# Kernel optimization log

Hardware: AMD Instinct MI355X
Metric: run time of the kernel (lower is better)

The kernel has to match this reference:

```python
import jax, jax.numpy as jnp
import numpy as np

N = 50000
E = 800000
IN = 128
HEADS = 4
C = 32  # out_features per head
HC = HEADS * C


def setup_inputs() -> dict:
    key = jax.random.key(0)
    ks = jax.random.split(key, 10)
    s_in = 1.0 / np.sqrt(IN)
    x = jax.random.normal(ks[0], (N, IN), dtype=jnp.float32)
    edge_index = jax.random.randint(ks[1], (2, E), 0, N, dtype=jnp.int64)
    Wq = jax.random.normal(ks[2], (IN, HC), dtype=jnp.float32) * s_in
    bq = jnp.zeros((HC,), dtype=jnp.float32)
    Wk = jax.random.normal(ks[3], (IN, HC), dtype=jnp.float32) * s_in
    bk = jnp.zeros((HC,), dtype=jnp.float32)
    Wv = jax.random.normal(ks[4], (IN, HC), dtype=jnp.float32) * s_in
    bv = jnp.zeros((HC,), dtype=jnp.float32)
    Wskip = jax.random.normal(ks[5], (IN, HC), dtype=jnp.float32) * s_in
    bskip = jnp.zeros((HC,), dtype=jnp.float32)
    return {"x": x, "edge_index": edge_index, "Wq": Wq, "bq": bq,
            "Wk": Wk, "bk": bk, "Wv": Wv, "bv": bv,
            "Wskip": Wskip, "bskip": bskip}


def reference(x, edge_index, Wq, bq, Wk, bk, Wv, bv, Wskip, bskip):
    src = edge_index[0]  # message source j
    dst = edge_index[1]  # message target i

    q = (x @ Wq + bq).reshape(N, HEADS, C)
    k = (x @ Wk + bk).reshape(N, HEADS, C)
    v = (x @ Wv + bv).reshape(N, HEADS, C)

    # per-edge attention logits: [E, H]
    logits = jnp.einsum('ehc,ehc->eh', q[dst], k[src]) / jnp.sqrt(
        jnp.asarray(C, dtype=x.dtype))

    # segment softmax over incoming edges of each target node
    seg_max = jax.ops.segment_max(logits, dst, num_segments=N)
    seg_max = jnp.where(jnp.isfinite(seg_max), seg_max, 0.0)
    expd = jnp.exp(logits - seg_max[dst])
    seg_sum = jax.ops.segment_sum(expd, dst, num_segments=N)
    alpha = expd / (seg_sum[dst] + 1e-16)  # [E, H]

    # scatter-add weighted values: [N, H, C]
    msgs = alpha[:, :, None] * v[src]
    out = jax.ops.segment_sum(msgs, dst, num_segments=N)
    out = out.reshape(N, HC) + (x @ Wskip + bskip)  # root/skip connection

    # LeakyReLU(negative_slope=0.2)
    return jnp.where(out >= 0, out, 0.2 * out)
```

## Files before the change

kernel.cpp:

```cpp
#include <hip/hip_runtime.h>

#define N_NODES 50000
#define E_EDGES 800000
#define IN_F 128
#define HC 128
#define ROWTILES 3125
#define GEMM_BLOCKS 500
#define HIST_BLOCKS 1563
#define CAP 64

typedef __attribute__((ext_vector_type(8))) short short8;
typedef __attribute__((ext_vector_type(4))) float floatx4;

__device__ __forceinline__ unsigned short f2bf(float f) {
    union { float f; unsigned u; } x; x.f = f;
    unsigned r = x.u + 0x7FFF + ((x.u >> 16) & 1);
    return (unsigned short)(r >> 16);
}
__device__ __forceinline__ float bflo(unsigned u) {
    union { unsigned u; float f; } c; c.u = u << 16; return c.f;
}
__device__ __forceinline__ float bfhi(unsigned u) {
    union { unsigned u; float f; } c; c.u = u & 0xFFFF0000u; return c.f;
}

__global__ __launch_bounds__(512) void gemm_hist(
    const float* __restrict__ x,
    const float* __restrict__ Wq, const float* __restrict__ Wk,
    const float* __restrict__ Wv, const float* __restrict__ Ws,
    const float* __restrict__ bq, const float* __restrict__ bk,
    const float* __restrict__ bv, const float* __restrict__ bs,
    unsigned short* __restrict__ q, unsigned short* __restrict__ k,
    unsigned short* __restrict__ v, float* __restrict__ out,
    const int* __restrict__ src, const int* __restrict__ dst,
    int* __restrict__ cnt, int* __restrict__ ssrc)
{
    if (blockIdx.x >= GEMM_BLOCKS) {
        int e = (blockIdx.x - GEMM_BLOCKS) * 512 + threadIdx.x;
        if (e < E_EDGES) {
            int d = dst[e];
            int r = atomicAdd(&cnt[d], 1);
            if (r < CAP) ssrc[(size_t)d * CAP + r] = src[e];
        }
        return;
    }
    __shared__ float As[16][132];
    __shared__ unsigned short Ep[3][16][136];

    const int tid = threadIdx.x;
    const int wv = tid >> 6;
    const int lane = tid & 63;
    const int cg = wv >> 1, hf = wv & 1;
    const int l16 = lane & 15, kh = lane >> 4;

    const float* Wsec = cg == 0 ? Wq : cg == 1 ? Wk : cg == 2 ? Wv : Ws;
    const float* bsec = cg == 0 ? bq : cg == 1 ? bk : cg == 2 ? bv : bs;

    short8 breg[4][4];
    float bias_[4];
#pragma unroll
    for (int n = 0; n < 4; n++) {
        const int col = (hf * 4 + n) * 16 + l16;
        bias_[n] = bsec[col];
#pragma unroll
        for (int ks = 0; ks < 4; ks++) {
            short8 bb;
#pragma unroll
            for (int j = 0; j < 8; j++)
                bb[j] = (short)f2bf(Wsec[(size_t)(ks * 32 + kh * 8 + j) * HC + col]);
            breg[n][ks] = bb;
        }
    }

    for (int rt = blockIdx.x; rt < ROWTILES; rt += GEMM_BLOCKS) {
        __syncthreads();
        {
            int r = tid >> 5, c4 = (tid & 31) * 4;
            float4 xv = *(const float4*)(x + (size_t)(rt * 16 + r) * IN_F + c4);
            *(float4*)&As[r][c4] = xv;
        }
        __syncthreads();

        short8 a[4];
#pragma unroll
        for (int ks = 0; ks < 4; ks++) {
            const float* ap = &As[l16][ks * 32 + kh * 8];
            float4 lo = *(const float4*)ap;
            float4 hi = *(const float4*)(ap + 4);
            short8 aa;
            aa[0] = (short)f2bf(lo.x); aa[1] = (short)f2bf(lo.y);
            aa[2] = (short)f2bf(lo.z); aa[3] = (short)f2bf(lo.w);
            aa[4] = (short)f2bf(hi.x); aa[5] = (short)f2bf(hi.y);
            aa[6] = (short)f2bf(hi.z); aa[7] = (short)f2bf(hi.w);
            a[ks] = aa;
        }

        floatx4 acc[4];
#pragma unroll
        for (int n = 0; n < 4; n++) acc[n] = {0.f, 0.f, 0.f, 0.f};
#pragma unroll
        for (int ks = 0; ks < 4; ks++)
#pragma unroll
            for (int n = 0; n < 4; n++)
                acc[n] = __builtin_amdgcn_mfma_f32_16x16x32_bf16(a[ks], breg[n][ks], acc[n], 0, 0, 0);

        if (cg < 3) {
#pragma unroll
            for (int n = 0; n < 4; n++) {
                const int c = (hf * 4 + n) * 16 + l16;
#pragma unroll
                for (int r = 0; r < 4; r++)
                    Ep[cg][kh * 4 + r][c] = f2bf(acc[n][r] + bias_[n]);
            }
        } else {
#pragma unroll
            for (int n = 0; n < 4; n++) {
                const int c = (hf * 4 + n) * 16 + l16;
#pragma unroll
                for (int r = 0; r < 4; r++)
                    out[(size_t)(rt * 16 + kh * 4 + r) * HC + c] = acc[n][r] + bias_[n];
            }
        }
        __syncthreads();
        for (int i = tid; i < 768; i += 512) {
            int cgi = i >> 8, wi = i & 255;
            int r = wi >> 4, cb = (wi & 15) * 8;
            uint4 val = *(const uint4*)&Ep[cgi][r][cb];
            unsigned short* dp = (cgi == 0 ? q : cgi == 1 ? k : v)
                                 + (size_t)(rt * 16 + r) * HC + cb;
            *(uint4*)dp = val;
        }
    }
}

__global__ __launch_bounds__(256) void node_attn(
    const unsigned short* __restrict__ q, const unsigned short* __restrict__ k,
    const unsigned short* __restrict__ v, const int* __restrict__ cnt,
    const int* __restrict__ ssrc, float* __restrict__ out)
{
    const int wave = (blockIdx.x * 256 + threadIdx.x) >> 6;
    if (wave >= N_NODES) return;
    const int lane = threadIdx.x & 63;
    const int node = wave;

    union { unsigned u; float f; } cv;
    const unsigned uq = *(const unsigned*)(q + (size_t)node * HC + lane * 2);
    cv.u = uq << 16;          float qx = cv.f;
    cv.u = uq & 0xFFFF0000u;  float qy = cv.f;

    float accx = 0.f, accy = 0.f, ssum = 0.f;
    int deg = __builtin_amdgcn_readfirstlane(cnt[node]);
    if (deg > CAP) deg = CAP;
    const int* sp = ssrc + (size_t)node * CAP;
    const float scale = 0.17677669529663687f;

    int e = 0;
    for (; e + 3 < deg; e += 4) {
        const int j0 = sp[e],     j1 = sp[e + 1];
        const int j2 = sp[e + 2], j3 = sp[e + 3];
        const unsigned uk0 = *(const unsigned*)(k + (size_t)j0 * HC + lane * 2);
        const unsigned uk1 = *(const unsigned*)(k + (size_t)j1 * HC + lane * 2);
        const unsigned uk2 = *(const unsigned*)(k + (size_t)j2 * HC + lane * 2);
        const unsigned uk3 = *(const unsigned*)(k + (size_t)j3 * HC + lane * 2);
        const unsigned uv0 = *(const unsigned*)(v + (size_t)j0 * HC + lane * 2);
        const unsigned uv1 = *(const unsigned*)(v + (size_t)j1 * HC + lane * 2);
        const unsigned uv2 = *(const unsigned*)(v + (size_t)j2 * HC + lane * 2);
        const unsigned uv3 = *(const unsigned*)(v + (size_t)j3 * HC + lane * 2);
        float p0, p1, p2, p3;
        { float kx, ky;
          cv.u = uk0 << 16; kx = cv.f; cv.u = uk0 & 0xFFFF0000u; ky = cv.f;
          p0 = qx * kx + qy * ky;
          cv.u = uk1 << 16; kx = cv.f; cv.u = uk1 & 0xFFFF0000u; ky = cv.f;
          p1 = qx * kx + qy * ky;
          cv.u = uk2 << 16; kx = cv.f; cv.u = uk2 & 0xFFFF0000u; ky = cv.f;
          p2 = qx * kx + qy * ky;
          cv.u = uk3 << 16; kx = cv.f; cv.u = uk3 & 0xFFFF0000u; ky = cv.f;
          p3 = qx * kx + qy * ky; }
#pragma unroll
        for (int off = 1; off <= 8; off <<= 1) {
            p0 += __shfl_xor(p0, off);
            p1 += __shfl_xor(p1, off);
            p2 += __shfl_xor(p2, off);
            p3 += __shfl_xor(p3, off);
        }
        const float w0 = __expf(p0 * scale);
        const float w1 = __expf(p1 * scale);
        const float w2 = __expf(p2 * scale);
        const float w3 = __expf(p3 * scale);
        { float vx, vy;
          cv.u = uv0 << 16; vx = cv.f; cv.u = uv0 & 0xFFFF0000u; vy = cv.f;
          accx += w0 * vx; accy += w0 * vy;
          cv.u = uv1 << 16; vx = cv.f; cv.u = uv1 & 0xFFFF0000u; vy = cv.f;
          accx += w1 * vx; accy += w1 * vy;
          cv.u = uv2 << 16; vx = cv.f; cv.u = uv2 & 0xFFFF0000u; vy = cv.f;
          accx += w2 * vx; accy += w2 * vy;
          cv.u = uv3 << 16; vx = cv.f; cv.u = uv3 & 0xFFFF0000u; vy = cv.f;
          accx += w3 * vx; accy += w3 * vy; }
        ssum += (w0 + w1) + (w2 + w3);
    }
    for (; e < deg; e++) {
        const int j0 = sp[e];
        const unsigned uk0 = *(const unsigned*)(k + (size_t)j0 * HC + lane * 2);
        const unsigned uv0 = *(const unsigned*)(v + (size_t)j0 * HC + lane * 2);
        float kx, ky;
        cv.u = uk0 << 16; kx = cv.f; cv.u = uk0 & 0xFFFF0000u; ky = cv.f;
        float p0 = qx * kx + qy * ky;
        p0 += __shfl_xor(p0, 1);
        p0 += __shfl_xor(p0, 2);
        p0 += __shfl_xor(p0, 4);
        p0 += __shfl_xor(p0, 8);
        const float w0 = __expf(p0 * scale);
        float vx, vy;
        cv.u = uv0 << 16; vx = cv.f; cv.u = uv0 & 0xFFFF0000u; vy = cv.f;
        accx += w0 * vx; accy += w0 * vy;
        ssum += w0;
    }

    const float inv = 1.0f / (ssum + 1e-16f);
    const float2 sk = *(const float2*)(out + (size_t)node * HC + lane * 2);
    float ox = accx * inv + sk.x;
    float oy = accy * inv + sk.y;
    ox = ox >= 0.f ? ox : 0.2f * ox;
    oy = oy >= 0.f ? oy : 0.2f * oy;
    *(float2*)(out + (size_t)node * HC + lane * 2) = make_float2(ox, oy);
}

extern "C" void kernel_launch(void* const* d_in, const int* in_sizes, int n_in,
                              void* d_out, int out_size, void* d_ws, size_t ws_size,
                              hipStream_t stream)
{
    const float* x    = (const float*)d_in[0];
    const int*   ei   = (const int*)d_in[1];
    const float* Wq   = (const float*)d_in[2];
    const float* bq   = (const float*)d_in[3];
    const float* Wk   = (const float*)d_in[4];
    const float* bk   = (const float*)d_in[5];
    const float* Wv   = (const float*)d_in[6];
    const float* bv   = (const float*)d_in[7];
    const float* Wsk  = (const float*)d_in[8];
    const float* bsk  = (const float*)d_in[9];
    float* out = (float*)d_out;

    char* w = (char*)d_ws;
    const size_t NFB = (size_t)N_NODES * HC * sizeof(unsigned short);
    unsigned short* q = (unsigned short*)w;            w += NFB;
    unsigned short* k = (unsigned short*)w;            w += NFB;
    unsigned short* v = (unsigned short*)w;            w += NFB;
    int* cnt  = (int*)w;                               w += N_NODES * sizeof(int);
    int* ssrc = (int*)w;

    const int* srcIdx = ei;
    const int* dstIdx = ei + E_EDGES;

    hipMemsetAsync(cnt, 0, N_NODES * sizeof(int), stream);
    gemm_hist<<<GEMM_BLOCKS + HIST_BLOCKS, 512, 0, stream>>>(
        x, Wq, Wk, Wv, Wsk, bq, bk, bv, bsk, q, k, v, out,
        srcIdx, dstIdx, cnt, ssrc);
    node_attn<<<(N_NODES * 64) / 256, 256, 0, stream>>>(q, k, v, cnt, ssrc, out);
}
```

Before: 157.4 us.

## Split histogram from GEMM and use per-wave swizzled LDS epilogue without block barriers

Separates the edge histogram/bucketing into its own kernel instead of sharing a launch with the projection GEMM. The GEMM now loads x rows straight from global memory rather than staging them in shared memory. Each wave stages its output tile in a private XOR-swizzled LDS region and writes it out with coalesced vector stores, which removes the block-wide __syncthreads. GEMM block count rises from 500 to 781. The cost is an extra kernel launch and the loss of overlap between hist and GEMM blocks inside one grid; x is also read redundantly by all eight waves.

```diff
diff --git a/kernel.cpp b/kernel.cpp
--- a/kernel.cpp
+++ b/kernel.cpp
@@ -5,7 +5,7 @@
 #define IN_F 128
 #define HC 128
 #define ROWTILES 3125
-#define GEMM_BLOCKS 500
+#define GEMM_BLOCKS 781
 #define HIST_BLOCKS 1563
 #define CAP 64
 
@@ -23,29 +23,31 @@
 __device__ __forceinline__ float bfhi(unsigned u) {
     union { unsigned u; float f; } c; c.u = u & 0xFFFF0000u; return c.f;
 }
-
-__global__ __launch_bounds__(512) void gemm_hist(
+__device__ __forceinline__ int swz16(int b) { return b ^ (((b >> 9)  & 3) << 5); }
+__device__ __forceinline__ int swz32(int b) { return b ^ (((b >> 10) & 3) << 5); }
+
+__global__ __launch_bounds__(512) void hist_k(
+    const int* __restrict__ src, const int* __restrict__ dst,
+    int* __restrict__ cnt, int* __restrict__ ssrc)
+{
+    int e = blockIdx.x * 512 + threadIdx.x;
+    if (e < E_EDGES) {
+        int d = dst[e];
+        int r = atomicAdd(&cnt[d], 1);
+        if (r < CAP) ssrc[(size_t)d * CAP + r] = src[e];
+    }
+}
+
+__global__ __launch_bounds__(512) void gemm_k(
     const float* __restrict__ x,
     const float* __restrict__ Wq, const float* __restrict__ Wk,
     const float* __restrict__ Wv, const float* __restrict__ Ws,
     const float* __restrict__ bq, const float* __restrict__ bk,
     const float* __restrict__ bv, const float* __restrict__ bs,
     unsigned short* __restrict__ q, unsigned short* __restrict__ k,
-    unsigned short* __restrict__ v, float* __restrict__ out,
-    const int* __restrict__ src, const int* __restrict__ dst,
-    int* __restrict__ cnt, int* __restrict__ ssrc)
-{
-    if (blockIdx.x >= GEMM_BLOCKS) {
-        int e = (blockIdx.x - GEMM_BLOCKS) * 512 + threadIdx.x;
-        if (e < E_EDGES) {
-            int d = dst[e];
-            int r = atomicAdd(&cnt[d], 1);
-            if (r < CAP) ssrc[(size_t)d * CAP + r] = src[e];
-        }
-        return;
-    }
-    __shared__ float As[16][132];
-    __shared__ unsigned short Ep[3][16][136];
+    unsigned short* __restrict__ v, float* __restrict__ out)
+{
+    __shared__ __align__(16) unsigned char lds[6 * 2048 + 2 * 4096];
 
     const int tid = threadIdx.x;
     const int wv = tid >> 6;
@@ -72,21 +74,19 @@
         }
     }
 
+    unsigned char* Eb = lds + wv * 2048;
+    unsigned char* Ef = lds + 12288 + hf * 4096;
+    unsigned short* dstb = (cg == 0) ? q : (cg == 1) ? k : v;
+
     for (int rt = blockIdx.x; rt < ROWTILES; rt += GEMM_BLOCKS) {
-        __syncthreads();
-        {
-            int r = tid >> 5, c4 = (tid & 31) * 4;
-            float4 xv = *(const float4*)(x + (size_t)(rt * 16 + r) * IN_F + c4);
-            *(float4*)&As[r][c4] = xv;
-        }
-        __syncthreads();
+        const size_t row = (size_t)rt * 16 + l16;
 
         short8 a[4];
 #pragma unroll
         for (int ks = 0; ks < 4; ks++) {
-            const float* ap = &As[l16][ks * 32 + kh * 8];
-            float4 lo = *(const float4*)ap;
-            float4 hi = *(const float4*)(ap + 4);
+            const float* p0 = x + row * IN_F + ks * 32 + kh * 8;
+            float4 lo = *(const float4*)p0;
+            float4 hi = *(const float4*)(p0 + 4);
             short8 aa;
             aa[0] = (short)f2bf(lo.x); aa[1] = (short)f2bf(lo.y);
             aa[2] = (short)f2bf(lo.z); aa[3] = (short)f2bf(lo.w);
@@ -107,28 +107,37 @@
         if (cg < 3) {
 #pragma unroll
             for (int n = 0; n < 4; n++) {
-                const int c = (hf * 4 + n) * 16 + l16;
-#pragma unroll
-                for (int r = 0; r < 4; r++)
-                    Ep[cg][kh * 4 + r][c] = f2bf(acc[n][r] + bias_[n]);
+#pragma unroll
+                for (int r = 0; r < 4; r++) {
+                    int boff = ((kh * 4 + r) * 64 + n * 16 + l16) * 2;
+                    *(unsigned short*)(Eb + swz16(boff)) = f2bf(acc[n][r] + bias_[n]);
+                }
+            }
+            unsigned short* gout = dstb + (size_t)rt * 16 * HC + hf * 64;
+#pragma unroll
+            for (int i = 0; i < 2; i++) {
+                int idx = i * 64 + lane;
+                uint4 val = *(const uint4*)(Eb + swz16(idx * 16));
+                int r = idx >> 3, cb = (idx & 7) * 8;
+                *(uint4*)(gout + r * HC + cb) = val;
             }
         } else {
 #pragma unroll
             for (int n = 0; n < 4; n++) {
-                const int c = (hf * 4 + n) * 16 + l16;
-#pragma unroll
-                for (int r = 0; r < 4; r++)
-                    out[(size_t)(rt * 16 + kh * 4 + r) * HC + c] = acc[n][r] + bias_[n];
-            }
-        }
-        __syncthreads();
-        for (int i = tid; i < 768; i += 512) {
-            int cgi = i >> 8, wi = i & 255;
-            int r = wi >> 4, cb = (wi & 15) * 8;
-            uint4 val = *(const uint4*)&Ep[cgi][r][cb];
-            unsigned short* dp = (cgi == 0 ? q : cgi == 1 ? k : v)
-                                 + (size_t)(rt * 16 + r) * HC + cb;
-            *(uint4*)dp = val;
+#pragma unroll
+                for (int r = 0; r < 4; r++) {
+                    int boff = ((kh * 4 + r) * 64 + n * 16 + l16) * 4;
+                    *(float*)(Ef + swz32(boff)) = acc[n][r] + bias_[n];
+                }
+            }
+            float* gout = out + (size_t)rt * 16 * HC + hf * 64;
+#pragma unroll
+            for (int i = 0; i < 4; i++) {
+                int idx = i * 64 + lane;
+                float4 val = *(const float4*)(Ef + swz32(idx * 16));
+                int r = idx >> 4, cb = (idx & 15) * 4;
+                *(float4*)(gout + r * HC + cb) = val;
+            }
         }
     }
 }
@@ -253,8 +262,8 @@
     const int* dstIdx = ei + E_EDGES;
 
     hipMemsetAsync(cnt, 0, N_NODES * sizeof(int), stream);
-    gemm_hist<<<GEMM_BLOCKS + HIST_BLOCKS, 512, 0, stream>>>(
-        x, Wq, Wk, Wv, Wsk, bq, bk, bv, bsk, q, k, v, out,
-        srcIdx, dstIdx, cnt, ssrc);
+    hist_k<<<HIST_BLOCKS, 512, 0, stream>>>(srcIdx, dstIdx, cnt, ssrc);
+    gemm_k<<<GEMM_BLOCKS, 512, 0, stream>>>(
+        x, Wq, Wk, Wv, Wsk, bq, bk, bv, bsk, q, k, v, out);
     node_attn<<<(N_NODES * 64) / 256, 256, 0, stream>>>(q, k, v, cnt, ssrc, out);
 }
```

Measured after the change: 167.8 us. 6.6% more time.
